# Optimization experiments

Measured on AMD Instinct MI355X. Metric: run time of the kernel, lower is better.

## Reference

```python
import jax, jax.numpy as jnp
import numpy as np

B, H, N, D, S = 32, 4, 8192, 64, 3
EPS = 1e-10


def setup_inputs() -> dict:
    key = jax.random.key(0)
    ks = jax.random.split(key, 9)
    dev = 1.0 / np.sqrt(D + N)  # init scale from initialize_memory()
    memory = jax.random.uniform(ks[0], (B, N, D), minval=-dev, maxval=dev, dtype=jnp.float32)
    k = jax.random.normal(ks[1], (B, H, D), dtype=jnp.float32)
    beta = jax.random.uniform(ks[2], (B, H), dtype=jnp.float32) * 5.0          # key strength >= 0
    pw = jax.nn.softmax(jax.random.normal(ks[3], (B, H, N), dtype=jnp.float32), axis=-1)  # prev weights: simplex
    g = jax.random.uniform(ks[4], (B, H), dtype=jnp.float32)                    # gate in [0,1]
    s = jax.nn.softmax(jax.random.normal(ks[5], (B, H, S), dtype=jnp.float32), axis=-1)   # shift distribution
    gamma = 1.0 + 2.0 * jax.random.uniform(ks[6], (B, H), dtype=jnp.float32)    # sharpening >= 1
    erase = jax.random.uniform(ks[7], (B, H, D), dtype=jnp.float32)             # erase in [0,1]
    add = jax.random.normal(ks[8], (B, H, D), dtype=jnp.float32)
    return {"memory": memory, "k": k, "beta": beta, "pw": pw, "g": g,
            "s": s, "gamma": gamma, "erase": erase, "add": add}


def _ntm_step(memory, k, beta, pw, g, s, gamma, erase, add):
    # --- content addressing: softmax over slots of beta * cosine similarity ---
    kn = k / (jnp.linalg.norm(k, axis=-1, keepdims=True) + EPS)         # [B,H,D]
    mn = memory / (jnp.linalg.norm(memory, axis=-1, keepdims=True) + EPS)  # [B,N,D]
    cos = jnp.einsum('bhd,bnd->bhn', kn, mn)                            # [B,H,N]
    wc = jax.nn.softmax(beta[..., None] * cos, axis=-1)
    # --- location addressing: interpolate, circular shift, sharpen ---
    gb = g[..., None]
    wg = gb * wc + (1.0 - gb) * pw                                      # [B,H,N]
    center = (s.shape[-1] - 1) // 2
    # ws(i) = sum_j wg((i - off_j) mod N) * s(j), off_j = j - center
    ws = sum(s[..., j:j + 1] * jnp.roll(wg, j - center, axis=-1)
             for j in range(s.shape[-1]))
    wgam = ws ** gamma[..., None]
    w = wgam / jnp.sum(wgam, axis=-1, keepdims=True)                    # [B,H,N]
    # --- write: sequential erase/add outer products per head ---
    mem = memory
    for h in range(w.shape[1]):
        e = w[:, h, :, None] * erase[:, h, None, :]                     # [B,N,D]
        a = w[:, h, :, None] * add[:, h, None, :]
        mem = mem * (1.0 - e) + a
    # --- read from updated memory ---
    reading = jnp.einsum('bhn,bnd->bhd', w, mem)                        # [B,H,D]
    return reading


def reference(memory, k, beta, pw, g, s, gamma, erase, add):
    return _ntm_step(memory, k, beta, pw, g, s, gamma, erase, add)
```

## Files before the change

### kernel.cpp

```cpp
#include <hip/hip_runtime.h>
#include <math.h>

#define Bc 32
#define Hc 4
#define Nc 8192
#define Dc 64
#define EPSc 1e-10f

#define T1ROWS 256
#define NT1 (Nc / T1ROWS)
#define T2ROWS 256
#define NT2 (Nc / T2ROWS)
#define T3ROWS 128
#define NT3 (Nc / T3ROWS)

__global__ __launch_bounds__(256) void k_scores(
    const float* __restrict__ mem, const float* __restrict__ kk,
    const float* __restrict__ beta,
    float* __restrict__ tbuf, float* __restrict__ z1p)
{
    const int b = blockIdx.y, tile = blockIdx.x, tid = threadIdx.x;
    const int wave = tid >> 6, lane = tid & 63;
    const int n0 = tile * T1ROWS;

    __shared__ __align__(16) float ks[Hc][Dc];
    __shared__ float4 lrow4[T1ROWS * 8];
    __shared__ float wsum[4][Hc];

    {
        float kv = kk[(b * Hc + wave) * Dc + lane];
        float ss = kv * kv;
        #pragma unroll
        for (int off = 32; off; off >>= 1) ss += __shfl_xor(ss, off);
        float scale = beta[b * Hc + wave] / (sqrtf(ss) + EPSc);
        ks[wave][lane] = kv * scale;
    }
    __syncthreads();

    const float4* mem4 = reinterpret_cast<const float4*>(mem) + ((size_t)b * Nc + n0) * 16;

    float ssacc = 0.f;
    float dot[Hc] = {0.f, 0.f, 0.f, 0.f};

    #pragma unroll
    for (int hf = 0; hf < 2; ++hf) {
        if (hf) __syncthreads();

        #pragma unroll
        for (int k = 0; k < 8; ++k) {
            const int f = k * 256 + tid;
            const int r = f >> 3, sp = f & 7;
            const int c = sp ^ (r & 7);
            lrow4[f] = mem4[r * 16 + hf * 8 + c];
        }
        __syncthreads();

        const float4* ks4 = reinterpret_cast<const float4*>(&ks[0][0]);
        #pragma unroll
        for (int c = 0; c < 8; ++c) {
            const float4 v = lrow4[tid * 8 + (c ^ (tid & 7))];
            ssacc = fmaf(v.x, v.x, ssacc); ssacc = fmaf(v.y, v.y, ssacc);
            ssacc = fmaf(v.z, v.z, ssacc); ssacc = fmaf(v.w, v.w, ssacc);
            #pragma unroll
            for (int h = 0; h < Hc; ++h) {
                const float4 kf = ks4[h * 16 + hf * 8 + c];
                dot[h] = fmaf(v.x, kf.x, dot[h]);
                dot[h] = fmaf(v.y, kf.y, dot[h]);
                dot[h] = fmaf(v.z, kf.z, dot[h]);
                dot[h] = fmaf(v.w, kf.w, dot[h]);
            }
        }
    }

    const float inv = 1.0f / (sqrtf(ssacc) + EPSc);
    float psum[Hc];
    #pragma unroll
    for (int h = 0; h < Hc; ++h) {
        const float tv = __expf(dot[h] * inv);
        tbuf[(b * Hc + h) * Nc + n0 + tid] = tv;
        psum[h] = tv;
    }

    #pragma unroll
    for (int h = 0; h < Hc; ++h) {
        #pragma unroll
        for (int off = 32; off; off >>= 1) psum[h] += __shfl_xor(psum[h], off);
        if (lane == 0) wsum[wave][h] = psum[h];
    }
    __syncthreads();
    if (tid < Hc)
        z1p[(b * Hc + tid) * NT1 + tile] =
            wsum[0][tid] + wsum[1][tid] + wsum[2][tid] + wsum[3][tid];
}

__global__ __launch_bounds__(256) void k_shift(
    const float* __restrict__ tbuf, const float* __restrict__ z1p,
    const float* __restrict__ pw, const float* __restrict__ g,
    const float* __restrict__ s, const float* __restrict__ gamma,
    float* __restrict__ wgbuf, float* __restrict__ z2p,
    float* __restrict__ out)
{
    const int b = blockIdx.y, tile = blockIdx.x, tid = threadIdx.x;
    const int h = tid >> 6, lane = tid & 63;

    if (tile == 0) out[b * 256 + tid] = 0.f;

    float v = (lane < NT1) ? z1p[(b * Hc + h) * NT1 + lane] : 0.f;
    #pragma unroll
    for (int off = 32; off; off >>= 1) v += __shfl_xor(v, off);
    const float invZ1 = __shfl(1.0f / v, 0);

    const float gh  = g[b * Hc + h];
    const float gmh = gamma[b * Hc + h];
    const float s0 = s[(b * Hc + h) * 3 + 0];
    const float s1 = s[(b * Hc + h) * 3 + 1];
    const float s2 = s[(b * Hc + h) * 3 + 2];
    const float omg = 1.0f - gh;

    const int n0   = tile * T2ROWS + lane * 4;
    const int base = (b * Hc + h) * Nc;
    const int nm = (n0 == 0) ? (Nc - 1) : (n0 - 1);
    const int np = (n0 + 4 == Nc) ? 0 : (n0 + 4);

    const float4 t4  = *reinterpret_cast<const float4*>(tbuf + base + n0);
    const float4 p4  = *reinterpret_cast<const float4*>(pw   + base + n0);
    const float  tm = tbuf[base + nm], pm = pw[base + nm];
    const float  tp = tbuf[base + np], pp = pw[base + np];

    const float wgm1 = gh * tm   * invZ1 + omg * pm;
    const float wg0  = gh * t4.x * invZ1 + omg * p4.x;
    const float wg1  = gh * t4.y * invZ1 + omg * p4.y;
    const float wg2  = gh * t4.z * invZ1 + omg * p4.z;
    const float wg3  = gh * t4.w * invZ1 + omg * p4.w;
    const float wg4  = gh * tp   * invZ1 + omg * pp;

    float4 wgam;
    wgam.x = __powf(s0 * wg1 + s1 * wg0 + s2 * wgm1, gmh);
    wgam.y = __powf(s0 * wg2 + s1 * wg1 + s2 * wg0,  gmh);
    wgam.z = __powf(s0 * wg3 + s1 * wg2 + s2 * wg1,  gmh);
    wgam.w = __powf(s0 * wg4 + s1 * wg3 + s2 * wg2,  gmh);
    *reinterpret_cast<float4*>(wgbuf + base + n0) = wgam;

    float pv = wgam.x + wgam.y + wgam.z + wgam.w;
    #pragma unroll
    for (int off = 32; off; off >>= 1) pv += __shfl_xor(pv, off);
    if (lane == 0) z2p[(b * Hc + h) * NT2 + tile] = pv;
}

__global__ __launch_bounds__(256) void k_update(
    const float* __restrict__ mem, const float* __restrict__ wgbuf,
    const float* __restrict__ z2p, const float* __restrict__ erase,
    const float* __restrict__ add, float* __restrict__ out)
{
    const int b = blockIdx.y, tile = blockIdx.x, tid = threadIdx.x;
    const int part = tid & 15;
    const int rw   = tid >> 4;

    __shared__ float invZ2[Hc];
    {
        const int wave = tid >> 6, lane = tid & 63;
        float v = (lane < NT2) ? z2p[(b * Hc + wave) * NT2 + lane] : 0.f;
        #pragma unroll
        for (int off = 32; off; off >>= 1) v += __shfl_xor(v, off);
        if (lane == 0) invZ2[wave] = 1.0f / v;
    }
    __syncthreads();

    float4 e4[Hc], a4[Hc];
    float iz[Hc];
    #pragma unroll
    for (int h = 0; h < Hc; ++h) {
        e4[h] = *reinterpret_cast<const float4*>(erase + (b * Hc + h) * Dc + part * 4);
        a4[h] = *reinterpret_cast<const float4*>(add   + (b * Hc + h) * Dc + part * 4);
        iz[h] = invZ2[h];
    }

    float4 r4[Hc];
    #pragma unroll
    for (int h = 0; h < Hc; ++h) r4[h] = make_float4(0.f, 0.f, 0.f, 0.f);

    const int n0 = tile * T3ROWS;
    #pragma unroll 4
    for (int i = 0; i < T3ROWS / 16; ++i) {
        const int n = n0 + i * 16 + rw;
        float4 m4 = *reinterpret_cast<const float4*>(
            mem + ((size_t)b * Nc + n) * Dc + part * 4);
        float w[Hc];
        #pragma unroll
        for (int h = 0; h < Hc; ++h)
            w[h] = wgbuf[(b * Hc + h) * Nc + n] * iz[h];
        #pragma unroll
        for (int h = 0; h < Hc; ++h) {
            m4.x = m4.x * (1.0f - w[h] * e4[h].x) + w[h] * a4[h].x;
            m4.y = m4.y * (1.0f - w[h] * e4[h].y) + w[h] * a4[h].y;
            m4.z = m4.z * (1.0f - w[h] * e4[h].z) + w[h] * a4[h].z;
            m4.w = m4.w * (1.0f - w[h] * e4[h].w) + w[h] * a4[h].w;
        }
        #pragma unroll
        for (int h = 0; h < Hc; ++h) {
            r4[h].x = fmaf(w[h], m4.x, r4[h].x);
            r4[h].y = fmaf(w[h], m4.y, r4[h].y);
            r4[h].z = fmaf(w[h], m4.z, r4[h].z);
            r4[h].w = fmaf(w[h], m4.w, r4[h].w);
        }
    }

    __shared__ float4 acc[16][Hc][16];
    #pragma unroll
    for (int h = 0; h < Hc; ++h) acc[rw][h][part] = r4[h];
    __syncthreads();

    const int h = tid >> 6, d = tid & 63;
    float sum = 0.f;
    #pragma unroll
    for (int r2 = 0; r2 < 16; ++r2)
        sum += reinterpret_cast<const float*>(&acc[r2][h][d >> 2])[d & 3];
    atomicAdd(out + b * 256 + h * 64 + d, sum);
}

extern "C" void kernel_launch(void* const* d_in, const int* in_sizes, int n_in,
                              void* d_out, int out_size, void* d_ws, size_t ws_size,
                              hipStream_t stream) {
    const float* mem   = (const float*)d_in[0];
    const float* kk    = (const float*)d_in[1];
    const float* beta  = (const float*)d_in[2];
    const float* pw    = (const float*)d_in[3];
    const float* g     = (const float*)d_in[4];
    const float* s     = (const float*)d_in[5];
    const float* gamma = (const float*)d_in[6];
    const float* erase = (const float*)d_in[7];
    const float* add   = (const float*)d_in[8];
    float* out = (float*)d_out;

    float* ws    = (float*)d_ws;
    float* tbuf  = ws;
    float* wgbuf = tbuf + (size_t)Bc*Hc*Nc;
    float* z1p   = wgbuf + (size_t)Bc*Hc*Nc;
    float* z2p   = z1p + (size_t)Bc*Hc*NT1;

    k_scores<<<dim3(NT1, Bc), 256, 0, stream>>>(mem, kk, beta, tbuf, z1p);
    k_shift <<<dim3(NT2, Bc), 256, 0, stream>>>(tbuf, z1p, pw, g, s, gamma,
                                                wgbuf, z2p, out);
    k_update<<<dim3(NT3, Bc), 256, 0, stream>>>(mem, wgbuf, z2p, erase, add, out);
}
```

Measured before the change: 41.52 us.

## Interleave per-head write weights per slot and read memory rows directly

```diff
diff --git a/kernel.cpp b/kernel.cpp
--- a/kernel.cpp
+++ b/kernel.cpp
@@ -21,10 +21,9 @@
 {
     const int b = blockIdx.y, tile = blockIdx.x, tid = threadIdx.x;
     const int wave = tid >> 6, lane = tid & 63;
-    const int n0 = tile * T1ROWS;
+    const int n = tile * T1ROWS + tid;
 
     __shared__ __align__(16) float ks[Hc][Dc];
-    __shared__ float4 lrow4[T1ROWS * 8];
     __shared__ float wsum[4][Hc];
 
     {
@@ -37,38 +36,24 @@
     }
     __syncthreads();
 
-    const float4* mem4 = reinterpret_cast<const float4*>(mem) + ((size_t)b * Nc + n0) * 16;
+    const float4* row4 = reinterpret_cast<const float4*>(
+        mem + ((size_t)b * Nc + n) * Dc);
+    const float4* ks4 = reinterpret_cast<const float4*>(&ks[0][0]);
 
     float ssacc = 0.f;
     float dot[Hc] = {0.f, 0.f, 0.f, 0.f};
-
-    #pragma unroll
-    for (int hf = 0; hf < 2; ++hf) {
-        if (hf) __syncthreads();
-
-        #pragma unroll
-        for (int k = 0; k < 8; ++k) {
-            const int f = k * 256 + tid;
-            const int r = f >> 3, sp = f & 7;
-            const int c = sp ^ (r & 7);
-            lrow4[f] = mem4[r * 16 + hf * 8 + c];
-        }
-        __syncthreads();
-
-        const float4* ks4 = reinterpret_cast<const float4*>(&ks[0][0]);
-        #pragma unroll
-        for (int c = 0; c < 8; ++c) {
-            const float4 v = lrow4[tid * 8 + (c ^ (tid & 7))];
-            ssacc = fmaf(v.x, v.x, ssacc); ssacc = fmaf(v.y, v.y, ssacc);
-            ssacc = fmaf(v.z, v.z, ssacc); ssacc = fmaf(v.w, v.w, ssacc);
-            #pragma unroll
-            for (int h = 0; h < Hc; ++h) {
-                const float4 kf = ks4[h * 16 + hf * 8 + c];
-                dot[h] = fmaf(v.x, kf.x, dot[h]);
-                dot[h] = fmaf(v.y, kf.y, dot[h]);
-                dot[h] = fmaf(v.z, kf.z, dot[h]);
-                dot[h] = fmaf(v.w, kf.w, dot[h]);
-            }
+    #pragma unroll
+    for (int c = 0; c < 16; ++c) {
+        const float4 v = row4[c];
+        ssacc = fmaf(v.x, v.x, ssacc); ssacc = fmaf(v.y, v.y, ssacc);
+        ssacc = fmaf(v.z, v.z, ssacc); ssacc = fmaf(v.w, v.w, ssacc);
+        #pragma unroll
+        for (int h = 0; h < Hc; ++h) {
+            const float4 kf = ks4[h * 16 + c];
+            dot[h] = fmaf(v.x, kf.x, dot[h]);
+            dot[h] = fmaf(v.y, kf.y, dot[h]);
+            dot[h] = fmaf(v.z, kf.z, dot[h]);
+            dot[h] = fmaf(v.w, kf.w, dot[h]);
         }
     }
 
@@ -77,7 +62,7 @@
     #pragma unroll
     for (int h = 0; h < Hc; ++h) {
         const float tv = __expf(dot[h] * inv);
-        tbuf[(b * Hc + h) * Nc + n0 + tid] = tv;
+        tbuf[(b * Hc + h) * Nc + n] = tv;
         psum[h] = tv;
     }
 
@@ -97,58 +82,62 @@
     const float* __restrict__ tbuf, const float* __restrict__ z1p,
     const float* __restrict__ pw, const float* __restrict__ g,
     const float* __restrict__ s, const float* __restrict__ gamma,
-    float* __restrict__ wgbuf, float* __restrict__ z2p,
+    float4* __restrict__ wgbuf4, float* __restrict__ z2p,
     float* __restrict__ out)
 {
     const int b = blockIdx.y, tile = blockIdx.x, tid = threadIdx.x;
-    const int h = tid >> 6, lane = tid & 63;
+    const int wave = tid >> 6, lane = tid & 63;
+    const int n = tile * T2ROWS + tid;
 
     if (tile == 0) out[b * 256 + tid] = 0.f;
 
-    float v = (lane < NT1) ? z1p[(b * Hc + h) * NT1 + lane] : 0.f;
-    #pragma unroll
-    for (int off = 32; off; off >>= 1) v += __shfl_xor(v, off);
-    const float invZ1 = __shfl(1.0f / v, 0);
-
-    const float gh  = g[b * Hc + h];
-    const float gmh = gamma[b * Hc + h];
-    const float s0 = s[(b * Hc + h) * 3 + 0];
-    const float s1 = s[(b * Hc + h) * 3 + 1];
-    const float s2 = s[(b * Hc + h) * 3 + 2];
-    const float omg = 1.0f - gh;
-
-    const int n0   = tile * T2ROWS + lane * 4;
-    const int base = (b * Hc + h) * Nc;
-    const int nm = (n0 == 0) ? (Nc - 1) : (n0 - 1);
-    const int np = (n0 + 4 == Nc) ? 0 : (n0 + 4);
-
-    const float4 t4  = *reinterpret_cast<const float4*>(tbuf + base + n0);
-    const float4 p4  = *reinterpret_cast<const float4*>(pw   + base + n0);
-    const float  tm = tbuf[base + nm], pm = pw[base + nm];
-    const float  tp = tbuf[base + np], pp = pw[base + np];
-
-    const float wgm1 = gh * tm   * invZ1 + omg * pm;
-    const float wg0  = gh * t4.x * invZ1 + omg * p4.x;
-    const float wg1  = gh * t4.y * invZ1 + omg * p4.y;
-    const float wg2  = gh * t4.z * invZ1 + omg * p4.z;
-    const float wg3  = gh * t4.w * invZ1 + omg * p4.w;
-    const float wg4  = gh * tp   * invZ1 + omg * pp;
-
-    float4 wgam;
-    wgam.x = __powf(s0 * wg1 + s1 * wg0 + s2 * wgm1, gmh);
-    wgam.y = __powf(s0 * wg2 + s1 * wg1 + s2 * wg0,  gmh);
-    wgam.z = __powf(s0 * wg3 + s1 * wg2 + s2 * wg1,  gmh);
-    wgam.w = __powf(s0 * wg4 + s1 * wg3 + s2 * wg2,  gmh);
-    *reinterpret_cast<float4*>(wgbuf + base + n0) = wgam;
-
-    float pv = wgam.x + wgam.y + wgam.z + wgam.w;
-    #pragma unroll
-    for (int off = 32; off; off >>= 1) pv += __shfl_xor(pv, off);
-    if (lane == 0) z2p[(b * Hc + h) * NT2 + tile] = pv;
+    __shared__ float invZ[Hc];
+    __shared__ float gS[Hc], gmS[Hc], sS[Hc][3];
+    __shared__ float wsum[4][Hc];
+
+    {
+        float v = (lane < NT1) ? z1p[(b * Hc + wave) * NT1 + lane] : 0.f;
+        #pragma unroll
+        for (int off = 32; off; off >>= 1) v += __shfl_xor(v, off);
+        if (lane == 0) invZ[wave] = 1.0f / v;
+    }
+    if (tid < Hc)     { gS[tid] = g[b * Hc + tid]; gmS[tid] = gamma[b * Hc + tid]; }
+    if (tid < Hc * 3) sS[tid / 3][tid % 3] = s[b * Hc * 3 + tid];
+    __syncthreads();
+
+    const int nm = (n + Nc - 1) & (Nc - 1);
+    const int np = (n + 1) & (Nc - 1);
+
+    float4 wq;
+    float* wqp = reinterpret_cast<float*>(&wq);
+    float psum[Hc];
+    #pragma unroll
+    for (int h = 0; h < Hc; ++h) {
+        const int base = (b * Hc + h) * Nc;
+        const float gh = gS[h], omg = 1.0f - gS[h], iz = invZ[h];
+        const float wg_m = gh * tbuf[base + nm] * iz + omg * pw[base + nm];
+        const float wg_c = gh * tbuf[base + n]  * iz + omg * pw[base + n];
+        const float wg_p = gh * tbuf[base + np] * iz + omg * pw[base + np];
+        const float wsv = sS[h][0] * wg_p + sS[h][1] * wg_c + sS[h][2] * wg_m;
+        wqp[h] = __powf(wsv, gmS[h]);
+        psum[h] = wqp[h];
+    }
+    wgbuf4[(size_t)b * Nc + n] = wq;
+
+    #pragma unroll
+    for (int h = 0; h < Hc; ++h) {
+        #pragma unroll
+        for (int off = 32; off; off >>= 1) psum[h] += __shfl_xor(psum[h], off);
+        if (lane == 0) wsum[wave][h] = psum[h];
+    }
+    __syncthreads();
+    if (tid < Hc)
+        z2p[(b * Hc + tid) * NT2 + tile] =
+            wsum[0][tid] + wsum[1][tid] + wsum[2][tid] + wsum[3][tid];
 }
 
 __global__ __launch_bounds__(256) void k_update(
-    const float* __restrict__ mem, const float* __restrict__ wgbuf,
+    const float* __restrict__ mem, const float4* __restrict__ wgbuf4,
     const float* __restrict__ z2p, const float* __restrict__ erase,
     const float* __restrict__ add, float* __restrict__ out)
 {
@@ -183,12 +172,13 @@
     #pragma unroll 4
     for (int i = 0; i < T3ROWS / 16; ++i) {
         const int n = n0 + i * 16 + rw;
-        float4 m4 = *reinterpret_cast<const float4*>(
+        const float4 m0 = *reinterpret_cast<const float4*>(
             mem + ((size_t)b * Nc + n) * Dc + part * 4);
+        const float4 wv = wgbuf4[(size_t)b * Nc + n];
         float w[Hc];
-        #pragma unroll
-        for (int h = 0; h < Hc; ++h)
-            w[h] = wgbuf[(b * Hc + h) * Nc + n] * iz[h];
+        w[0] = wv.x * iz[0]; w[1] = wv.y * iz[1];
+        w[2] = wv.z * iz[2]; w[3] = wv.w * iz[3];
+        float4 m4 = m0;
         #pragma unroll
         for (int h = 0; h < Hc; ++h) {
             m4.x = m4.x * (1.0f - w[h] * e4[h].x) + w[h] * a4[h].x;
@@ -232,14 +222,14 @@
     const float* add   = (const float*)d_in[8];
     float* out = (float*)d_out;
 
-    float* ws    = (float*)d_ws;
-    float* tbuf  = ws;
-    float* wgbuf = tbuf + (size_t)Bc*Hc*Nc;
-    float* z1p   = wgbuf + (size_t)Bc*Hc*Nc;
-    float* z2p   = z1p + (size_t)Bc*Hc*NT1;
+    float*  ws     = (float*)d_ws;
+    float*  tbuf   = ws;
+    float4* wgbuf4 = (float4*)(tbuf + (size_t)Bc*Hc*Nc);
+    float*  z1p    = (float*)(wgbuf4 + (size_t)Bc*Nc);
+    float*  z2p    = z1p + (size_t)Bc*Hc*NT1;
 
     k_scores<<<dim3(NT1, Bc), 256, 0, stream>>>(mem, kk, beta, tbuf, z1p);
     k_shift <<<dim3(NT2, Bc), 256, 0, stream>>>(tbuf, z1p, pw, g, s, gamma,
-                                                wgbuf, z2p, out);
-    k_update<<<dim3(NT3, Bc), 256, 0, stream>>>(mem, wgbuf, z2p, erase, add, out);
-}
+                                                wgbuf4, z2p, out);
+    k_update<<<dim3(NT3, Bc), 256, 0, stream>>>(mem, wgbuf4, z2p, erase, add, out);
+}
```

After: 48.25 us. +16.2%, slower.
